# Performance work log

Hardware: AMD Instinct MI355X
Metric: run time of the kernel (lower is better)

Reference implementation:

```python
import jax, jax.numpy as jnp
import numpy as np

B, R, N, M, K = 4, 4, 4096, 64, 3
F_NUM = 512
KN = K * N


def _block(x, Ws, bs):
    """SO-Net PointResNet: 1x1 convs + ReLU; last layer sees concat(input, hidden)."""
    h = x
    for W, b in zip(Ws[:-1], bs[:-1]):
        h = jax.nn.relu(jnp.einsum('oc,bcn->bon', W, h) + b[None, :, None])
    h = jnp.concatenate([x, h], axis=1)
    return jax.nn.relu(jnp.einsum('oc,bcn->bon', Ws[-1], h) + bs[-1][None, :, None])


def _forward(x, intensity, node, node_knn_I, fpW, fpB, gpW, gpB):
    # --- som.query_topk: k nearest SOM nodes per point ---
    xd = jax.lax.stop_gradient(x)
    dist = jnp.sum((xd[:, :, :, None] - node[:, :, None, :]) ** 2, axis=1)      # B,N,M
    _, topk = jax.lax.top_k(-dist, K)                                           # B,N,K
    min_idx = topk.transpose(0, 2, 1).reshape(B, KN)                            # B,KN (k copies stacked)
    mask = jax.nn.one_hot(min_idx, M, dtype=jnp.float32)                        # B,KN,M
    mask_row_max = jnp.max(mask, axis=1) > 0                                    # B,M  node has >=1 point
    mask_row_sum = jnp.sum(mask, axis=1)                                        # B,M  points per node

    x_stack = jnp.tile(x, (1, 1, K))                                            # B,2,KN
    cluster_mean = jnp.einsum('bcn,bnm->bcm', jax.lax.stop_gradient(x_stack), mask) \
                   / (mask_row_sum[:, None, :] + 1e-5)                          # B,2,M (detached)

    # --- rotation group (2x2 rotations at angles 2*pi*r/R) ---
    theta = 2.0 * jnp.pi * jnp.arange(R, dtype=jnp.float32) / R
    c, s = jnp.cos(theta), jnp.sin(theta)
    rot = jnp.stack([jnp.stack([c, -s], -1), jnp.stack([s, c], -1)], -2)        # R,2,2

    x_rot = jnp.einsum('rij,bjn->brin', rot, x_stack)                           # B,R,2,KN
    node_rot = jnp.einsum('rij,bjm->brim', rot, cluster_mean)                   # B,R,2,M
    centers = jnp.take_along_axis(node_rot, min_idx[:, None, None, :], axis=3)  # B,R,2,KN
    x_dec = jax.lax.stop_gradient(x_rot - centers).reshape(B * R, 2, KN)

    # --- first PointResNet over all B*R rotation copies ---
    feat = _block(x_dec, fpW, fpB)                                              # BR,128,KN

    # --- index_max scatter-max per SOM cluster (value of argmax == segment max) ---
    seg = jnp.tile(min_idx[:, None, :], (1, R, 1)).reshape(B * R, KN)
    segmax = jax.vmap(lambda f, sgi: jax.ops.segment_max(f.T, sgi, num_segments=M).T)(feat, seg)
    rowmax = jnp.tile(mask_row_max[:, None, :], (1, R, 1)).reshape(B * R, M)
    pooled = jnp.where(rowmax[:, None, :], segmax, feat[:, :, 0:1])             # BR,128,M (empty -> gather idx 0)

    # --- final PointResNet over SOM nodes, then max over nodes and rotations ---
    g_in = jnp.concatenate([node_rot.reshape(B * R, 2, M), pooled], axis=1)     # BR,130,M
    out = _block(g_in, gpW, gpB)                                                # BR,F,M
    return out.reshape(B, R, F_NUM, M).max(axis=3).max(axis=1)                  # B,F


def setup_inputs() -> dict:
    key = jax.random.key(0)
    ks = jax.random.split(key, 24)
    d = {}
    d['x'] = jax.random.normal(ks[0], (B, 2, N), jnp.float32)
    d['intensity'] = jax.random.uniform(ks[1], (B, 1, N), jnp.float32)
    d['node'] = jax.random.normal(ks[2], (B, 2, M), jnp.float32)
    d['node_knn_I'] = jax.random.randint(ks[3], (B, M, 1), 0, M)
    dims_fp = [(64, 2), (64, 64), (128, 64), (128, 130)]      # PointResNet(2,[64,64,128,128])
    dims_gp = [(256, 130), (256, 256), (512, 256), (F_NUM, 642)]  # PointResNet(130,[256,256,512,F])
    i = 4
    for name, dims in (('fp', dims_fp), ('gp', dims_gp)):
        for j, (o, ci) in enumerate(dims):
            d[f'{name}_W{j}'] = jax.random.normal(ks[i], (o, ci), jnp.float32) / np.sqrt(ci).astype(np.float32)
            d[f'{name}_b{j}'] = jnp.zeros((o,), jnp.float32)
            i += 1
    return d


def reference(x, intensity, node, node_knn_I,
              fp_W0, fp_b0, fp_W1, fp_b1, fp_W2, fp_b2, fp_W3, fp_b3,
              gp_W0, gp_b0, gp_W1, gp_b1, gp_W2, gp_b2, gp_W3, gp_b3):
    return _forward(x, intensity, node, node_knn_I,
                    [fp_W0, fp_W1, fp_W2, fp_W3], [fp_b0, fp_b1, fp_b2, fp_b3],
                    [gp_W0, gp_W1, gp_W2, gp_W3], [gp_b0, gp_b1, gp_b2, gp_b3])
```

## Files before the change

kernel.cpp:

```cpp
#include <hip/hip_runtime.h>
#include <stdint.h>

#define BB 4
#define RR 4
#define NN 4096
#define MM 64
#define KK 3
#define KNN 12288
#define BRR 16
#define FF 512

typedef short bf16x8 __attribute__((ext_vector_type(8)));
typedef float f32x4 __attribute__((ext_vector_type(4)));

__device__ __forceinline__ float bf2f(unsigned int u) {
  union { unsigned int i; float f; } v; v.i = u << 16; return v.f;
}
__device__ __forceinline__ unsigned short f2bf(float f) {
  union { float f; unsigned int i; } v; v.f = f;
  unsigned int x = v.i;
  return (unsigned short)((x + 0x7fffu + ((x >> 16) & 1u)) >> 16);
}
__device__ __forceinline__ unsigned int cvtpk(float a, float b) {
  unsigned int r;
  asm("v_cvt_pk_bf16_f32 %0, %1, %2" : "=v"(r) : "v"(a), "v"(b));
  return r;
}
__device__ __forceinline__ float ldf(const void* p, long i, int isbf) {
  if (isbf) return bf2f(((const unsigned short*)p)[i]);
  return ((const float*)p)[i];
}
__device__ __forceinline__ int hsw(int col, int so) { return col * 72  + (so ^ (col & 24)); }
__device__ __forceinline__ int csw(int col, int so) { return col * 168 + (so ^ (col & 24)); }

struct WPtrs { const void* p[16]; };

__global__ __launch_bounds__(256) void k_front(
    const void* __restrict__ x, const void* __restrict__ node, WPtrs wp,
    int* __restrict__ flag, unsigned short* __restrict__ Wb,
    unsigned short* __restrict__ fW3p, float* __restrict__ Fb,
    int* __restrict__ idx, float* __restrict__ csum, int* __restrict__ blkcnt) {
  __shared__ int bad;
  __shared__ float nd[2][64];
  __shared__ float cs[192];
  int tid = threadIdx.x;
  if (tid == 0) bad = 0;
  __syncthreads();
  {
    const unsigned short* xs = (const unsigned short*)x;
    int cnt = 0;
    for (int i = tid; i < 1024; i += 256) {
      unsigned short u = xs[i * 2];
      int e = (u >> 7) & 0xFF;
      if (e >= 0x90 || (e > 0 && e <= 0x50)) ++cnt;
    }
    atomicAdd(&bad, cnt);
  }
  __syncthreads();
  int isbf = (bad < 100) ? 1 : 0;
  if (blockIdx.x == 0 && tid == 0) flag[0] = isbf;

  if (blockIdx.x < 298) {
    const int e0=4096, e1=12288, e2=28928, e3=62208, e4=127744, e5=258816, e6=587520;
    int t8 = blockIdx.x * 256 + tid;
    if (t8 < 73440) {
      int base = t8 * 8;
      int s, segb;
      if      (base < e0) { s=0; segb=0;  }
      else if (base < e1) { s=1; segb=e0; }
      else if (base < e2) { s=2; segb=e1; }
      else if (base < e3) { s=3; segb=e2; }
      else if (base < e4) { s=4; segb=e3; }
      else if (base < e5) { s=5; segb=e4; }
      else                { s=6; segb=e5; }
      int local = base - segb;
      union { bf16x8 v; unsigned int u[4]; } ov;
      if (isbf) {
        ov.v = *(const bf16x8*)((const unsigned short*)wp.p[s] + local);
      } else {
        const float4* fp = (const float4*)((const float*)wp.p[s] + local);
        float4 f0 = fp[0], f1 = fp[1];
        ov.u[0] = cvtpk(f0.x, f0.y); ov.u[1] = cvtpk(f0.z, f0.w);
        ov.u[2] = cvtpk(f1.x, f1.y); ov.u[3] = cvtpk(f1.z, f1.w);
      }
      *(bf16x8*)(Wb + base) = ov.v;
    } else if (t8 < 76000) {
      int v = t8 - 73440;
      int base = v * 8;
      int o = v / 20, c = (v - o * 20) * 8;
      union { bf16x8 vv; unsigned short s8[8]; } ov;
#pragma unroll
      for (int j = 0; j < 8; ++j) {
        int cc = c + j;
        unsigned short u = 0;
        if (cc < 130) {
          long si = (long)o * 130 + cc;
          if (isbf) u = ((const unsigned short*)wp.p[2])[si];
          else      u = f2bf(((const float*)wp.p[2])[si]);
        }
        ov.s8[j] = u;
      }
      *(bf16x8*)(fW3p + base) = ov.vv;
    } else if (t8 < 76256) {
      int l = (t8 - 76000) * 8;
      const void* src; int off;
      if      (l < 128)  { src = wp.p[7];  off = 0;    }
      else if (l < 192)  { src = wp.p[8];  off = 128;  }
      else if (l < 256)  { src = wp.p[9];  off = 192;  }
      else if (l < 384)  { src = wp.p[10]; off = 256;  }
      else if (l < 512)  { src = wp.p[11]; off = 384;  }
      else if (l < 768)  { src = wp.p[12]; off = 512;  }
      else if (l < 1024) { src = wp.p[13]; off = 768;  }
      else if (l < 1536) { src = wp.p[14]; off = 1024; }
      else               { src = wp.p[15]; off = 1536; }
#pragma unroll
      for (int j = 0; j < 8; ++j) Fb[l + j] = ldf(src, l + j - off, isbf);
    }
    return;
  }
  int bi = blockIdx.x - 298;
  int b = bi >> 4;
  int n = ((bi & 15) << 8) + tid;
  if (tid < 128) nd[tid >> 6][tid & 63] = ldf(node, b * 128 + tid, isbf);
  if (tid < 192) cs[tid] = 0.f;
  __syncthreads();
  float x0 = ldf(x, b * 8192 + n, isbf);
  float x1 = ldf(x, b * 8192 + 4096 + n, isbf);
  float d0 = 1e30f, d1 = 1e30f, d2 = 1e30f;
  int m0 = 0, m1 = 0, m2 = 0;
#pragma unroll 8
  for (int m = 0; m < 64; ++m) {
    float dx = x0 - nd[0][m];
    float dy = x1 - nd[1][m];
    float d = __fmul_rn(dx, dx) + __fmul_rn(dy, dy);
    if (d < d0)      { d2=d1; m2=m1; d1=d0; m1=m0; d0=d; m0=m; }
    else if (d < d1) { d2=d1; m2=m1; d1=d;  m1=m; }
    else if (d < d2) { d2=d;  m2=m; }
  }
  long base = ((long)b * NN + n) * 3;
  idx[base] = m0; idx[base + 1] = m1; idx[base + 2] = m2;
  atomicAdd(&cs[m0*3+0], x0); atomicAdd(&cs[m0*3+1], x1); atomicAdd(&cs[m0*3+2], 1.f);
  atomicAdd(&cs[m1*3+0], x0); atomicAdd(&cs[m1*3+1], x1); atomicAdd(&cs[m1*3+2], 1.f);
  atomicAdd(&cs[m2*3+0], x0); atomicAdd(&cs[m2*3+1], x1); atomicAdd(&cs[m2*3+2], 1.f);
  __syncthreads();
  if (tid < 192) atomicAdd(&csum[b * 192 + tid], cs[tid]);
  if (tid < 64) blkcnt[bi * 64 + tid] = (int)cs[tid*3 + 2];
}

__global__ __launch_bounds__(256) void k_scatter2(
    const float* __restrict__ csum, const int* __restrict__ blkcnt,
    const int* __restrict__ idx, int* __restrict__ sorted,
    float* __restrict__ noderot, int* __restrict__ rowflag) {
  __shared__ int scnt[64];
  __shared__ int soff[64];
  __shared__ int lc[64];
  int tid = threadIdx.x;
  int blk = blockIdx.x;
  int b = blk >> 4, chunk = blk & 15;
  if (tid < 64) scnt[tid] = (int)csum[b*192 + tid*3 + 2];
  __syncthreads();
  if (tid < 64) {
    int m = tid, acc = 0;
    for (int mm = 0; mm < m; ++mm) acc += scnt[mm];
    for (int c = 0; c < chunk; ++c) acc += blkcnt[(b*16 + c)*64 + m];
    soff[m] = acc;
    lc[m] = 0;
    if (chunk == 0) {
      float s0 = csum[b*192 + m*3], s1 = csum[b*192 + m*3 + 1], cc = csum[b*192 + m*3 + 2];
      float mx = s0 / (cc + 1e-5f);
      float my = s1 / (cc + 1e-5f);
      rowflag[b*64 + m] = (cc > 0.f) ? 1 : 0;
      for (int r = 0; r < 4; ++r) {
        float th = 1.5707964f * (float)r;
        float cr = cosf(th), sr = sinf(th);
        noderot[((b*4 + r)*2 + 0)*64 + m] = cr*mx - sr*my;
        noderot[((b*4 + r)*2 + 1)*64 + m] = sr*mx + cr*my;
      }
    }
  }
  __syncthreads();
  int n = ((blk & 15) << 8) + tid;
#pragma unroll
  for (int kk = 0; kk < 3; ++kk) {
    int m = idx[((long)b * NN + n) * 3 + kk];
    int pos = atomicAdd(&lc[m], 1);
    sorted[b * KNN + soff[m] + pos] = (m << 12) | n;
  }
}

__global__ __launch_bounds__(256) void k_fused(
    const void* __restrict__ x, const int* __restrict__ sorted,
    const int* __restrict__ idx, const float* __restrict__ noderot,
    const int* __restrict__ flag, const unsigned short* __restrict__ Wb,
    const unsigned short* __restrict__ fW3p, const float* __restrict__ Fb,
    unsigned int* __restrict__ pooled, float* __restrict__ feat0) {
  __shared__ unsigned short Cs[64 * 168];
  __shared__ unsigned short Hs[64 * 72];
  __shared__ int mcol[64];
  const unsigned short* fW1 = Wb;
  const unsigned short* fW2 = Wb + 4096;
  int isbf = flag[0];
  int tid = threadIdx.x, lane = tid & 63, wv = tid >> 6;
  int quad = lane >> 4, lr = lane & 15;
  int br = blockIdx.y, b = br >> 2, r = br & 3;
  int o1 = wv * 16;
  if (tid < 64) {
    int e = sorted[b * KNN + blockIdx.x * 64 + tid];
    int m = e >> 12, n = e & 4095;
    int isz = (n == 0 && m == idx[(long)b * NN * 3]) ? 256 : 0;
    mcol[tid] = m | isz;
    float x0 = ldf(x, b*8192 + n, isbf), x1 = ldf(x, b*8192 + 4096 + n, isbf);
    float th = 1.5707964f * (float)r;
    float cr = cosf(th), sr = sinf(th);
    float xd0 = (cr*x0 - sr*x1) - noderot[(br*2 + 0)*64 + m];
    float xd1 = (sr*x0 + cr*x1) - noderot[(br*2 + 1)*64 + m];
    *(unsigned int*)&Cs[csw(tid, 0)] = cvtpk(xd0, xd1);
  }
  for (int z = tid; z < 960; z += 256) {
    int col = z / 15, l = 130 + (z - col * 15) * 2;
    *(unsigned int*)&Cs[csw(col, l)] = 0u;
  }
  __syncthreads();
  {
    int col = tid & 63, og = (tid >> 6) << 4;
    unsigned int xu = *(unsigned int*)&Cs[csw(col, 0)];
    float fx0 = bf2f(xu & 0xffff), fx1 = bf2f(xu >> 16);
    const float2* w2 = (const float2*)Fb;
    float hv[16];
#pragma unroll
    for (int j = 0; j < 16; ++j) {
      int o = og + j;
      float2 w = w2[o];
      float h = Fb[128 + o] + w.x * fx0 + w.y * fx1;
      hv[j] = fmaxf(h, 0.f);
    }
    union { bf16x8 v; unsigned int u[4]; } o8[2];
#pragma unroll
    for (int j = 0; j < 16; j += 2) o8[j >> 3].u[(j & 7) >> 1] = cvtpk(hv[j], hv[j+1]);
    *(bf16x8*)&Hs[hsw(col, og)]     = o8[0].v;
    *(bf16x8*)&Hs[hsw(col, og + 8)] = o8[1].v;
  }
  __syncthreads();
  {
    f32x4 acc[4];
#pragma unroll
    for (int nt = 0; nt < 4; ++nt)
      acc[nt] = (f32x4){Fb[192 + o1 + quad*4], Fb[192 + o1 + quad*4 + 1],
                        Fb[192 + o1 + quad*4 + 2], Fb[192 + o1 + quad*4 + 3]};
#pragma unroll
    for (int ks2 = 0; ks2 < 2; ++ks2) {
      bf16x8 a = *(const bf16x8*)(fW1 + (o1 + lr)*64 + ks2*32 + quad*8);
#pragma unroll
      for (int nt = 0; nt < 4; ++nt) {
        bf16x8 bf = *(bf16x8*)&Hs[hsw(nt*16 + lr, ks2*32 + quad*8)];
        acc[nt] = __builtin_amdgcn_mfma_f32_16x16x32_bf16(a, bf, acc[nt], 0, 0, 0);
      }
    }
    __syncthreads();
#pragma unroll
    for (int nt = 0; nt < 4; ++nt) {
      int col = nt*16 + lr;
      unsigned int lo = cvtpk(fmaxf(acc[nt][0], 0.f), fmaxf(acc[nt][1], 0.f));
      unsigned int hi = cvtpk(fmaxf(acc[nt][2], 0.f), fmaxf(acc[nt][3], 0.f));
      *(unsigned long long*)&Hs[hsw(col, o1 + quad*4)] =
          (unsigned long long)lo | ((unsigned long long)hi << 32);
    }
  }
  __syncthreads();
#pragma unroll
  for (int p2 = 0; p2 < 2; ++p2) {
    int o0 = p2*64 + o1;
    f32x4 acc[4];
#pragma unroll
    for (int nt = 0; nt < 4; ++nt)
      acc[nt] = (f32x4){Fb[256 + o0 + quad*4], Fb[256 + o0 + quad*4 + 1],
                        Fb[256 + o0 + quad*4 + 2], Fb[256 + o0 + quad*4 + 3]};
#pragma unroll
    for (int ks2 = 0; ks2 < 2; ++ks2) {
      bf16x8 a = *(const bf16x8*)(fW2 + (o0 + lr)*64 + ks2*32 + quad*8);
#pragma unroll
      for (int nt = 0; nt < 4; ++nt) {
        bf16x8 bf = *(bf16x8*)&Hs[hsw(nt*16 + lr, ks2*32 + quad*8)];
        acc[nt] = __builtin_amdgcn_mfma_f32_16x16x32_bf16(a, bf, acc[nt], 0, 0, 0);
      }
    }
#pragma unroll
    for (int nt = 0; nt < 4; ++nt) {
      int col = nt*16 + lr;
      int o = o0 + quad*4;
      unsigned int w0 = cvtpk(fmaxf(acc[nt][0], 0.f), fmaxf(acc[nt][1], 0.f));
      unsigned int w1 = cvtpk(fmaxf(acc[nt][2], 0.f), fmaxf(acc[nt][3], 0.f));
      *(unsigned int*)&Cs[csw(col, 2 + o)] = w0;
      *(unsigned int*)&Cs[csw(col, 4 + o)] = w1;
    }
  }
  __syncthreads();
  f32x4 acc3[2][4];
#pragma unroll
  for (int p3 = 0; p3 < 2; ++p3) {
    int o0 = p3*64 + o1;
#pragma unroll
    for (int nt = 0; nt < 4; ++nt)
      acc3[p3][nt] = (f32x4){Fb[384 + o0 + quad*4], Fb[384 + o0 + quad*4 + 1],
                             Fb[384 + o0 + quad*4 + 2], Fb[384 + o0 + quad*4 + 3]};
#pragma unroll
    for (int ks5 = 0; ks5 < 5; ++ks5) {
      bf16x8 a = *(const bf16x8*)(fW3p + (o0 + lr)*160 + ks5*32 + quad*8);
#pragma unroll
      for (int nt = 0; nt < 4; ++nt) {
        bf16x8 bf = *(bf16x8*)&Cs[csw(nt*16 + lr, ks5*32 + quad*8)];
        acc3[p3][nt] = __builtin_amdgcn_mfma_f32_16x16x32_bf16(a, bf, acc3[p3][nt], 0, 0, 0);
      }
    }
  }
  __syncthreads();
#pragma unroll
  for (int p3 = 0; p3 < 2; ++p3) {
    int o0 = p3*64 + o1;
#pragma unroll
    for (int nt = 0; nt < 4; ++nt) {
      int col = nt*16 + lr;
      unsigned int lo = cvtpk(fmaxf(acc3[p3][nt][0], 0.f), fmaxf(acc3[p3][nt][1], 0.f));
      unsigned int hi = cvtpk(fmaxf(acc3[p3][nt][2], 0.f), fmaxf(acc3[p3][nt][3], 0.f));
      *(unsigned long long*)&Cs[csw(col, o0 + quad*4)] =
          (unsigned long long)lo | ((unsigned long long)hi << 32);
    }
  }
  __syncthreads();
  {
    int opair = tid & 63, h = tid >> 6;
    int o0 = opair * 2;
    int c0 = h * 16;
    int curm = mcol[c0] & 255;
    unsigned int vlo = 0u, vhi = 0u;
    for (int c = c0; c < c0 + 16; ++c) {
      int mc = mcol[c];
      int mm = mc & 255;
      unsigned int u = *(unsigned int*)&Cs[csw(c, o0)];
      if (mm != curm) {
        atomicMax(&pooled[(((long)br*64 + curm) << 7) + o0],     vlo);
        atomicMax(&pooled[(((long)br*64 + curm) << 7) + o0 + 1], vhi);
        curm = mm; vlo = vhi = 0u;
      }
      vlo = max(vlo, u << 16);
      vhi = max(vhi, u & 0xffff0000u);
      if (mc & 256) {
        feat0[br*128 + o0]     = __uint_as_float(u << 16);
        feat0[br*128 + o0 + 1] = __uint_as_float(u & 0xffff0000u);
      }
    }
    atomicMax(&pooled[(((long)br*64 + curm) << 7) + o0],     vlo);
    atomicMax(&pooled[(((long)br*64 + curm) << 7) + o0 + 1], vhi);
  }
}

template<int OT, int KW, int KMAIN, bool REM2, int DSTR, int DOFF, int EPI>
__device__ __forceinline__ void gp_layer(
    const unsigned short* __restrict__ W, const float* __restrict__ bias,
    const unsigned short* Bs, int bstr, unsigned short* Ds,
    int wv, int quad, int lr, int b, unsigned int* __restrict__ outmax) {
  f32x4 acc[OT];
#pragma unroll
  for (int ot = 0; ot < OT; ++ot) {
    int o0 = (wv * OT + ot) * 16;
    acc[ot] = (f32x4){bias[o0 + quad*4], bias[o0 + quad*4 + 1],
                      bias[o0 + quad*4 + 2], bias[o0 + quad*4 + 3]};
  }
  const unsigned short* brow = Bs + lr * bstr;
  for (int ks = 0; ks < KMAIN; ks += 32) {
    bf16x8 bf = *(const bf16x8*)(brow + ks + quad*8);
    bf16x8 a[OT];
#pragma unroll
    for (int ot = 0; ot < OT; ++ot) {
      const unsigned short* arow = W + (long)((wv * OT + ot) * 16 + lr) * KW;
      if constexpr ((KW % 8) == 0) {
        a[ot] = *(const bf16x8*)(arow + ks + quad*8);
      } else {
        union { bf16x8 v; unsigned int u[4]; } au;
        const unsigned int* ap = (const unsigned int*)(arow + ks + quad*8);
        au.u[0] = ap[0]; au.u[1] = ap[1]; au.u[2] = ap[2]; au.u[3] = ap[3];
        a[ot] = au.v;
      }
    }
#pragma unroll
    for (int ot = 0; ot < OT; ++ot)
      acc[ot] = __builtin_amdgcn_mfma_f32_16x16x32_bf16(a[ot], bf, acc[ot], 0, 0, 0);
  }
  if constexpr (REM2) {
    unsigned int bu = *(const unsigned int*)(brow + KMAIN);
    float b0 = bf2f(bu & 0xffff), b1 = bf2f(bu >> 16);
#pragma unroll
    for (int ot = 0; ot < OT; ++ot) {
#pragma unroll
      for (int rr = 0; rr < 4; ++rr) {
        int o = (wv * OT + ot) * 16 + quad*4 + rr;
        unsigned int wu = *(const unsigned int*)(W + (long)o * KW + KMAIN);
        acc[ot][rr] += bf2f(wu & 0xffff) * b0 + bf2f(wu >> 16) * b1;
      }
    }
  }
#pragma unroll
  for (int ot = 0; ot < OT; ++ot) {
    int o0 = (wv * OT + ot) * 16;
    if constexpr (EPI == 0) {
      unsigned int lo = cvtpk(fmaxf(acc[ot][0], 0.f), fmaxf(acc[ot][1], 0.f));
      unsigned int hi = cvtpk(fmaxf(acc[ot][2], 0.f), fmaxf(acc[ot][3], 0.f));
      unsigned short* op = Ds + lr * DSTR + DOFF + o0 + quad*4;
      if constexpr ((DOFF & 3) == 0) {
        *(unsigned long long*)op = (unsigned long long)lo | ((unsigned long long)hi << 32);
      } else {
        *(unsigned int*)op       = lo;
        *(unsigned int*)(op + 2) = hi;
      }
    } else {
#pragma unroll
      for (int rr = 0; rr < 4; ++rr) {
        float v = fmaxf(acc[ot][rr], 0.f);
        v = fmaxf(v, __shfl_xor(v, 1, 64));
        v = fmaxf(v, __shfl_xor(v, 2, 64));
        v = fmaxf(v, __shfl_xor(v, 4, 64));
        v = fmaxf(v, __shfl_xor(v, 8, 64));
        if (lr == 0)
          atomicMax(&outmax[b * FF + o0 + quad*4 + rr], __float_as_uint(v));
      }
    }
  }
}

__global__ __launch_bounds__(1024) void k_gp(
    const unsigned int* __restrict__ pooled, const float* __restrict__ feat0,
    const int* __restrict__ rowflag, const float* __restrict__ noderot,
    const unsigned short* __restrict__ Wb, const float* __restrict__ Fb,
    const int* __restrict__ flag, int* __restrict__ tick,
    unsigned int* __restrict__ outmax, void* __restrict__ out) {
  __shared__ unsigned short G3[16 * 648];
  __shared__ unsigned short H1[16 * 264];
  __shared__ unsigned short H2[16 * 264];
  __shared__ int lastf;
  const unsigned short* gW0 = Wb + 28928;
  const unsigned short* gW1 = Wb + 62208;
  const unsigned short* gW2 = Wb + 127744;
  const unsigned short* gW3 = Wb + 258816;
  int tid = threadIdx.x, lane = tid & 63, wv = tid >> 6;
  int quad = lane >> 4, lr = lane & 15;
  int c0 = blockIdx.x * 16;
  int br = c0 >> 6, b = br >> 2;
  {
    int j = tid >> 6, oq = (tid & 63) << 1;
    int col = c0 + j, m = col & 63;
    int fl = rowflag[b * 64 + m];
    float v0 = __uint_as_float(pooled[((long)col << 7) + oq]);
    float v1 = __uint_as_float(pooled[((long)col << 7) + oq + 1]);
    if (!fl) { v0 = feat0[br * 128 + oq]; v1 = feat0[br * 128 + oq + 1]; }
    *(unsigned int*)&G3[j * 648 + 2 + oq] = cvtpk(v0, v1);
    if (tid < 32) {
      int jj = tid >> 1, o = tid & 1;
      int mm = (c0 + jj) & 63;
      G3[jj * 648 + o] = f2bf(noderot[(br * 2 + o) * 64 + mm]);
    }
  }
  __syncthreads();
  gp_layer<1, 130, 128, true,  264, 0,   0>(gW0, Fb + 512,  G3, 648, H1, wv, quad, lr, b, outmax);
  __syncthreads();
  gp_layer<1, 256, 256, false, 264, 0,   0>(gW1, Fb + 768,  H1, 264, H2, wv, quad, lr, b, outmax);
  __syncthreads();
  gp_layer<2, 256, 256, false, 648, 130, 0>(gW2, Fb + 1024, H2, 264, G3, wv, quad, lr, b, outmax);
  __syncthreads();
  gp_layer<2, 642, 640, true,  0,   0,   1>(gW3, Fb + 1536, G3, 648, nullptr, wv, quad, lr, b, outmax);
  __threadfence();
  if (tid == 0) lastf = (atomicAdd(tick, 1) == 63) ? 1 : 0;
  __syncthreads();
  if (lastf) {
    int isbf = flag[0];
    for (int t = tid; t < 2048; t += 1024) {
      unsigned int u = atomicMax(&outmax[t], 0u);
      float v = __uint_as_float(u);
      if (isbf) ((unsigned short*)out)[t] = f2bf(v);
      else      ((float*)out)[t] = v;
    }
  }
}

extern "C" void kernel_launch(void* const* d_in, const int* in_sizes, int n_in,
                              void* d_out, int out_size, void* d_ws, size_t ws_size,
                              hipStream_t stream) {
  const void* x    = d_in[0];
  const void* node = d_in[2];

  char* ws = (char*)d_ws;
  int*            flag    = (int*)(ws + 0);
  int*            tick    = (int*)(ws + 128);
  float*          csum    = (float*)(ws + 256);
  unsigned int*   outmax  = (unsigned int*)(ws + 3328);
  unsigned int*   pooled  = (unsigned int*)(ws + 11520);
  int*            idx     = (int*)(ws + 535808);
  int*            blkcnt  = (int*)(ws + 732416);
  float*          noderot = (float*)(ws + 766208);
  int*            rowflag = (int*)(ws + 774400);
  int*            sorted  = (int*)(ws + 775424);
  float*          feat0   = (float*)(ws + 972032);
  unsigned short* fW3p    = (unsigned short*)(ws + 980224);
  float*          Fb      = (float*)(ws + 1021184);
  unsigned short* Wb      = (unsigned short*)(ws + 3355904);

  hipMemsetAsync(ws, 0, 535808, stream);

  WPtrs wp;
  wp.p[0]=d_in[6];  wp.p[1]=d_in[8];  wp.p[2]=d_in[10];
  wp.p[3]=d_in[12]; wp.p[4]=d_in[14]; wp.p[5]=d_in[16]; wp.p[6]=d_in[18];
  wp.p[7]=d_in[4];
  wp.p[8]=d_in[5];  wp.p[9]=d_in[7];  wp.p[10]=d_in[9]; wp.p[11]=d_in[11];
  wp.p[12]=d_in[13]; wp.p[13]=d_in[15]; wp.p[14]=d_in[17]; wp.p[15]=d_in[19];

  k_front<<<362, 256, 0, stream>>>(x, node, wp, flag, Wb, fW3p, Fb, idx, csum, blkcnt);
  k_scatter2<<<64, 256, 0, stream>>>(csum, blkcnt, idx, sorted, noderot, rowflag);
  k_fused<<<dim3(192, 16), 256, 0, stream>>>(x, sorted, idx, noderot, flag,
                                             Wb, fW3p, Fb, pooled, feat0);
  k_gp<<<64, 1024, 0, stream>>>(pooled, feat0, rowflag, noderot, Wb, Fb,
                                flag, tick, outmax, d_out);
}
```

Before: 202.8 us.

## Prefetch gp weights into cache from fused kernel and batch weight loads

The fused first-stage kernel now has each block read a slice of the later-layer weight buffer and discard the result. This is meant to warm the L2/MALL cache before the gp layers run. The gp_layer inner loop is restructured to load A and B fragments for four k-steps before issuing their MFMAs, so more global loads are in flight at once. This raises register pressure. The loop assumes KMAIN/32 is a multiple of 4, otherwise it reads past the range.

```diff
diff --git a/kernel.cpp b/kernel.cpp
--- a/kernel.cpp
+++ b/kernel.cpp
@@ -204,6 +204,18 @@
   int quad = lane >> 4, lr = lane & 15;
   int br = blockIdx.y, b = br >> 2, r = br & 3;
   int o1 = wv * 16;
+  {
+    unsigned int wacc = 0;
+#pragma unroll
+    for (int i = 0; i < 2; ++i) {
+      int off = 28928 + blockIdx.x * 2912 + i * 2048 + tid * 8;
+      if (off < 587520) {
+        const unsigned int* p = (const unsigned int*)(Wb + off);
+        wacc ^= p[0] ^ p[1] ^ p[2] ^ p[3];
+      }
+    }
+    asm volatile("" :: "v"(wacc));
+  }
   if (tid < 64) {
     int e = sorted[b * KNN + blockIdx.x * 64 + tid];
     int m = e >> 12, n = e & 4095;
@@ -367,24 +379,33 @@
                       bias[o0 + quad*4 + 2], bias[o0 + quad*4 + 3]};
   }
   const unsigned short* brow = Bs + lr * bstr;
-  for (int ks = 0; ks < KMAIN; ks += 32) {
-    bf16x8 bf = *(const bf16x8*)(brow + ks + quad*8);
-    bf16x8 a[OT];
-#pragma unroll
-    for (int ot = 0; ot < OT; ++ot) {
-      const unsigned short* arow = W + (long)((wv * OT + ot) * 16 + lr) * KW;
-      if constexpr ((KW % 8) == 0) {
-        a[ot] = *(const bf16x8*)(arow + ks + quad*8);
-      } else {
-        union { bf16x8 v; unsigned int u[4]; } au;
-        const unsigned int* ap = (const unsigned int*)(arow + ks + quad*8);
-        au.u[0] = ap[0]; au.u[1] = ap[1]; au.u[2] = ap[2]; au.u[3] = ap[3];
-        a[ot] = au.v;
-      }
-    }
-#pragma unroll
-    for (int ot = 0; ot < OT; ++ot)
-      acc[ot] = __builtin_amdgcn_mfma_f32_16x16x32_bf16(a[ot], bf, acc[ot], 0, 0, 0);
+  constexpr int NS = KMAIN / 32;
+#pragma unroll 1
+  for (int c = 0; c < NS; c += 4) {
+    bf16x8 bfv[4];
+    bf16x8 av[4][OT];
+#pragma unroll
+    for (int j = 0; j < 4; ++j) {
+      int ks = (c + j) * 32;
+      bfv[j] = *(const bf16x8*)(brow + ks + quad*8);
+#pragma unroll
+      for (int ot = 0; ot < OT; ++ot) {
+        const unsigned short* arow = W + (long)((wv * OT + ot) * 16 + lr) * KW;
+        if constexpr ((KW % 8) == 0) {
+          av[j][ot] = *(const bf16x8*)(arow + ks + quad*8);
+        } else {
+          union { bf16x8 v; unsigned int u[4]; } au;
+          const unsigned int* ap = (const unsigned int*)(arow + ks + quad*8);
+          au.u[0] = ap[0]; au.u[1] = ap[1]; au.u[2] = ap[2]; au.u[3] = ap[3];
+          av[j][ot] = au.v;
+        }
+      }
+    }
+#pragma unroll
+    for (int j = 0; j < 4; ++j)
+#pragma unroll
+      for (int ot = 0; ot < OT; ++ot)
+        acc[ot] = __builtin_amdgcn_mfma_f32_16x16x32_bf16(av[j][ot], bfv[j], acc[ot], 0, 0, 0);
   }
   if constexpr (REM2) {
     unsigned int bu = *(const unsigned int*)(brow + KMAIN);
```

Measured after the change: 207.0 us. +2.0%, slower.

## Split fused GP MLP kernel into per-layer GEMM launches with wider grids

Applied to the files above, without the earlier changes.

Replaces the single 64-block, 1024-thread kernel that ran all four GP layers in shared memory with four separate GEMM kernel launches, each spread over a 2D grid of output-channel tiles and point tiles. Intermediate activations now round-trip through global workspace buffers, and layer 3 recomputes the pooled-feature gather instead of reading it from shared memory. The aim is more parallelism and better CU occupancy across the GPU, at the cost of extra launches, global memory traffic, and weight reloads per block.

```diff
diff --git a/kernel.cpp b/kernel.cpp
--- a/kernel.cpp
+++ b/kernel.cpp
@@ -354,129 +354,134 @@
   }
 }
 
-template<int OT, int KW, int KMAIN, bool REM2, int DSTR, int DOFF, int EPI>
-__device__ __forceinline__ void gp_layer(
+template<int KW, int KWP, int KMAIN, bool REM2, bool GIN, int INSTR, int HOFF,
+         int NT, int EPI, int NBLK>
+__global__ __launch_bounds__(256) void k_gemm(
     const unsigned short* __restrict__ W, const float* __restrict__ bias,
-    const unsigned short* Bs, int bstr, unsigned short* Ds,
-    int wv, int quad, int lr, int b, unsigned int* __restrict__ outmax) {
-  f32x4 acc[OT];
-#pragma unroll
-  for (int ot = 0; ot < OT; ++ot) {
-    int o0 = (wv * OT + ot) * 16;
-    acc[ot] = (f32x4){bias[o0 + quad*4], bias[o0 + quad*4 + 1],
-                      bias[o0 + quad*4 + 2], bias[o0 + quad*4 + 3]};
-  }
-  const unsigned short* brow = Bs + lr * bstr;
-  for (int ks = 0; ks < KMAIN; ks += 32) {
-    bf16x8 bf = *(const bf16x8*)(brow + ks + quad*8);
-    bf16x8 a[OT];
-#pragma unroll
-    for (int ot = 0; ot < OT; ++ot) {
-      const unsigned short* arow = W + (long)((wv * OT + ot) * 16 + lr) * KW;
-      if constexpr ((KW % 8) == 0) {
-        a[ot] = *(const bf16x8*)(arow + ks + quad*8);
-      } else {
-        union { bf16x8 v; unsigned int u[4]; } au;
-        const unsigned int* ap = (const unsigned int*)(arow + ks + quad*8);
-        au.u[0] = ap[0]; au.u[1] = ap[1]; au.u[2] = ap[2]; au.u[3] = ap[3];
-        a[ot] = au.v;
-      }
-    }
-#pragma unroll
-    for (int ot = 0; ot < OT; ++ot)
-      acc[ot] = __builtin_amdgcn_mfma_f32_16x16x32_bf16(a[ot], bf, acc[ot], 0, 0, 0);
-  }
-  if constexpr (REM2) {
-    unsigned int bu = *(const unsigned int*)(brow + KMAIN);
-    float b0 = bf2f(bu & 0xffff), b1 = bf2f(bu >> 16);
-#pragma unroll
-    for (int ot = 0; ot < OT; ++ot) {
-#pragma unroll
-      for (int rr = 0; rr < 4; ++rr) {
-        int o = (wv * OT + ot) * 16 + quad*4 + rr;
-        unsigned int wu = *(const unsigned int*)(W + (long)o * KW + KMAIN);
-        acc[ot][rr] += bf2f(wu & 0xffff) * b0 + bf2f(wu >> 16) * b1;
-      }
-    }
-  }
-#pragma unroll
-  for (int ot = 0; ot < OT; ++ot) {
-    int o0 = (wv * OT + ot) * 16;
-    if constexpr (EPI == 0) {
-      unsigned int lo = cvtpk(fmaxf(acc[ot][0], 0.f), fmaxf(acc[ot][1], 0.f));
-      unsigned int hi = cvtpk(fmaxf(acc[ot][2], 0.f), fmaxf(acc[ot][3], 0.f));
-      unsigned short* op = Ds + lr * DSTR + DOFF + o0 + quad*4;
-      if constexpr ((DOFF & 3) == 0) {
-        *(unsigned long long*)op = (unsigned long long)lo | ((unsigned long long)hi << 32);
-      } else {
-        *(unsigned int*)op       = lo;
-        *(unsigned int*)(op + 2) = hi;
-      }
-    } else {
-#pragma unroll
-      for (int rr = 0; rr < 4; ++rr) {
-        float v = fmaxf(acc[ot][rr], 0.f);
-        v = fmaxf(v, __shfl_xor(v, 1, 64));
-        v = fmaxf(v, __shfl_xor(v, 2, 64));
-        v = fmaxf(v, __shfl_xor(v, 4, 64));
-        v = fmaxf(v, __shfl_xor(v, 8, 64));
-        if (lr == 0)
-          atomicMax(&outmax[b * FF + o0 + quad*4 + rr], __float_as_uint(v));
-      }
-    }
-  }
-}
-
-__global__ __launch_bounds__(1024) void k_gp(
     const unsigned int* __restrict__ pooled, const float* __restrict__ feat0,
     const int* __restrict__ rowflag, const float* __restrict__ noderot,
-    const unsigned short* __restrict__ Wb, const float* __restrict__ Fb,
-    const int* __restrict__ flag, int* __restrict__ tick,
-    unsigned int* __restrict__ outmax, void* __restrict__ out) {
-  __shared__ unsigned short G3[16 * 648];
-  __shared__ unsigned short H1[16 * 264];
-  __shared__ unsigned short H2[16 * 264];
+    const unsigned short* __restrict__ Bg, unsigned short* __restrict__ Out,
+    int OSTR, unsigned int* __restrict__ outmax,
+    const int* __restrict__ flag, int* __restrict__ tick, void* __restrict__ out) {
+  __shared__ __align__(16) unsigned short Bs[NT * 16 * KWP];
   __shared__ int lastf;
-  const unsigned short* gW0 = Wb + 28928;
-  const unsigned short* gW1 = Wb + 62208;
-  const unsigned short* gW2 = Wb + 127744;
-  const unsigned short* gW3 = Wb + 258816;
   int tid = threadIdx.x, lane = tid & 63, wv = tid >> 6;
   int quad = lane >> 4, lr = lane & 15;
-  int c0 = blockIdx.x * 16;
-  int br = c0 >> 6, b = br >> 2;
-  {
-    int j = tid >> 6, oq = (tid & 63) << 1;
-    int col = c0 + j, m = col & 63;
-    int fl = rowflag[b * 64 + m];
-    float v0 = __uint_as_float(pooled[((long)col << 7) + oq]);
-    float v1 = __uint_as_float(pooled[((long)col << 7) + oq + 1]);
-    if (!fl) { v0 = feat0[br * 128 + oq]; v1 = feat0[br * 128 + oq + 1]; }
-    *(unsigned int*)&G3[j * 648 + 2 + oq] = cvtpk(v0, v1);
-    if (tid < 32) {
-      int jj = tid >> 1, o = tid & 1;
-      int mm = (c0 + jj) & 63;
-      G3[jj * 648 + o] = f2bf(noderot[(br * 2 + o) * 64 + mm]);
-    }
-  }
-  __syncthreads();
-  gp_layer<1, 130, 128, true,  264, 0,   0>(gW0, Fb + 512,  G3, 648, H1, wv, quad, lr, b, outmax);
-  __syncthreads();
-  gp_layer<1, 256, 256, false, 264, 0,   0>(gW1, Fb + 768,  H1, 264, H2, wv, quad, lr, b, outmax);
-  __syncthreads();
-  gp_layer<2, 256, 256, false, 648, 130, 0>(gW2, Fb + 1024, H2, 264, G3, wv, quad, lr, b, outmax);
-  __syncthreads();
-  gp_layer<2, 642, 640, true,  0,   0,   1>(gW3, Fb + 1536, G3, 648, nullptr, wv, quad, lr, b, outmax);
-  __threadfence();
-  if (tid == 0) lastf = (atomicAdd(tick, 1) == 63) ? 1 : 0;
-  __syncthreads();
-  if (lastf) {
-    int isbf = flag[0];
-    for (int t = tid; t < 2048; t += 1024) {
-      unsigned int u = atomicMax(&outmax[t], 0u);
-      float v = __uint_as_float(u);
-      if (isbf) ((unsigned short*)out)[t] = f2bf(v);
-      else      ((float*)out)[t] = v;
+  int p0 = blockIdx.x * (NT * 16);
+  int br = p0 >> 6, b = br >> 2;
+  if constexpr (GIN) {
+    for (int i = tid; i < NT * 256; i += 256) {
+      int j = i >> 4, g = i & 15;
+      int col = p0 + j, m = col & 63;
+      int fl = rowflag[b * 64 + m];
+      int o8 = g * 8;
+      unsigned int wq[4];
+#pragma unroll
+      for (int q = 0; q < 4; ++q) {
+        float v0, v1;
+        if (fl) {
+          v0 = __uint_as_float(pooled[((long)col << 7) + o8 + q*2]);
+          v1 = __uint_as_float(pooled[((long)col << 7) + o8 + q*2 + 1]);
+        } else {
+          v0 = feat0[br * 128 + o8 + q*2];
+          v1 = feat0[br * 128 + o8 + q*2 + 1];
+        }
+        wq[q] = cvtpk(v0, v1);
+      }
+#pragma unroll
+      for (int q = 0; q < 4; ++q)
+        *(unsigned int*)&Bs[j * KWP + 2 + o8 + q*2] = wq[q];
+    }
+    if (tid < NT * 32) {
+      int j = tid >> 1, o = tid & 1;
+      Bs[j * KWP + o] = f2bf(noderot[(br * 2 + o) * 64 + ((p0 + j) & 63)]);
+    }
+  }
+  if constexpr (INSTR > 0) {
+    constexpr int NG = INSTR / 8;
+    for (int i = tid; i < NT * 16 * NG; i += 256) {
+      int j = i / NG, g = i - j * NG;
+      union { bf16x8 v; unsigned int u[4]; } t;
+      t.v = *(const bf16x8*)&Bg[(long)(p0 + j) * INSTR + g * 8];
+      if constexpr ((HOFF % 8) == 0) {
+        *(bf16x8*)&Bs[j * KWP + HOFF + g * 8] = t.v;
+      } else {
+#pragma unroll
+        for (int q = 0; q < 4; ++q)
+          *(unsigned int*)&Bs[j * KWP + HOFF + g * 8 + q*2] = t.u[q];
+      }
+    }
+  }
+  __syncthreads();
+  int o0 = blockIdx.y * 64 + wv * 16;
+  f32x4 acc[NT];
+#pragma unroll
+  for (int nt = 0; nt < NT; ++nt)
+    acc[nt] = (f32x4){bias[o0 + quad*4], bias[o0 + quad*4 + 1],
+                      bias[o0 + quad*4 + 2], bias[o0 + quad*4 + 3]};
+  const unsigned short* arow = W + (long)(o0 + lr) * KW;
+  for (int ks = 0; ks < KMAIN; ks += 32) {
+    bf16x8 a;
+    if constexpr ((KW % 8) == 0) {
+      a = *(const bf16x8*)(arow + ks + quad*8);
+    } else {
+      union { bf16x8 v; unsigned int u[4]; } au;
+      const unsigned int* ap = (const unsigned int*)(arow + ks + quad*8);
+      au.u[0] = ap[0]; au.u[1] = ap[1]; au.u[2] = ap[2]; au.u[3] = ap[3];
+      a = au.v;
+    }
+#pragma unroll
+    for (int nt = 0; nt < NT; ++nt) {
+      bf16x8 bf = *(bf16x8*)&Bs[(nt*16 + lr) * KWP + ks + quad*8];
+      acc[nt] = __builtin_amdgcn_mfma_f32_16x16x32_bf16(a, bf, acc[nt], 0, 0, 0);
+    }
+  }
+  if constexpr (REM2) {
+#pragma unroll
+    for (int rr = 0; rr < 4; ++rr) {
+      int o = o0 + quad*4 + rr;
+      unsigned int wu = *(const unsigned int*)(W + (long)o * KW + KMAIN);
+      float w0 = bf2f(wu & 0xffff), w1 = bf2f(wu >> 16);
+#pragma unroll
+      for (int nt = 0; nt < NT; ++nt) {
+        unsigned int bu = *(unsigned int*)&Bs[(nt*16 + lr) * KWP + KMAIN];
+        acc[nt][rr] += w0 * bf2f(bu & 0xffff) + w1 * bf2f(bu >> 16);
+      }
+    }
+  }
+  if constexpr (EPI == 0) {
+#pragma unroll
+    for (int nt = 0; nt < NT; ++nt) {
+      unsigned int lo = cvtpk(fmaxf(acc[nt][0], 0.f), fmaxf(acc[nt][1], 0.f));
+      unsigned int hi = cvtpk(fmaxf(acc[nt][2], 0.f), fmaxf(acc[nt][3], 0.f));
+      unsigned short* op = Out + (long)(p0 + nt*16 + lr) * OSTR + o0 + quad*4;
+      *(unsigned long long*)op = (unsigned long long)lo | ((unsigned long long)hi << 32);
+    }
+  } else {
+#pragma unroll
+    for (int rr = 0; rr < 4; ++rr) {
+      float v = acc[0][rr];
+#pragma unroll
+      for (int nt = 1; nt < NT; ++nt) v = fmaxf(v, acc[nt][rr]);
+      v = fmaxf(v, 0.f);
+      v = fmaxf(v, __shfl_xor(v, 1, 64));
+      v = fmaxf(v, __shfl_xor(v, 2, 64));
+      v = fmaxf(v, __shfl_xor(v, 4, 64));
+      v = fmaxf(v, __shfl_xor(v, 8, 64));
+      if (lr == 0)
+        atomicMax(&outmax[b * FF + o0 + quad*4 + rr], __float_as_uint(v));
+    }
+    __threadfence();
+    if (tid == 0) lastf = (atomicAdd(tick, 1) == NBLK - 1) ? 1 : 0;
+    __syncthreads();
+    if (lastf) {
+      int isbf = flag[0];
+      for (int t = tid; t < 2048; t += 256) {
+        unsigned int u = atomicMax(&outmax[t], 0u);
+        float v = __uint_as_float(u);
+        if (isbf) ((unsigned short*)out)[t] = f2bf(v);
+        else      ((float*)out)[t] = v;
+      }
     }
   }
 }
@@ -501,6 +506,9 @@
   float*          feat0   = (float*)(ws + 972032);
   unsigned short* fW3p    = (unsigned short*)(ws + 980224);
   float*          Fb      = (float*)(ws + 1021184);
+  unsigned short* Hg3     = (unsigned short*)(ws + 1048576);
+  unsigned short* Hg1     = (unsigned short*)(ws + 2307328);
+  unsigned short* Hg2     = (unsigned short*)(ws + 2831616);
   unsigned short* Wb      = (unsigned short*)(ws + 3355904);
 
   hipMemsetAsync(ws, 0, 535808, stream);
@@ -512,10 +520,29 @@
   wp.p[8]=d_in[5];  wp.p[9]=d_in[7];  wp.p[10]=d_in[9]; wp.p[11]=d_in[11];
   wp.p[12]=d_in[13]; wp.p[13]=d_in[15]; wp.p[14]=d_in[17]; wp.p[15]=d_in[19];
 
+  const unsigned short* gW0 = Wb + 28928;
+  const unsigned short* gW1 = Wb + 62208;
+  const unsigned short* gW2 = Wb + 127744;
+  const unsigned short* gW3 = Wb + 258816;
+
   k_front<<<362, 256, 0, stream>>>(x, node, wp, flag, Wb, fW3p, Fb, idx, csum, blkcnt);
   k_scatter2<<<64, 256, 0, stream>>>(csum, blkcnt, idx, sorted, noderot, rowflag);
   k_fused<<<dim3(192, 16), 256, 0, stream>>>(x, sorted, idx, noderot, flag,
                                              Wb, fW3p, Fb, pooled, feat0);
-  k_gp<<<64, 1024, 0, stream>>>(pooled, feat0, rowflag, noderot, Wb, Fb,
-                                flag, tick, outmax, d_out);
-}
+  k_gemm<130, 136, 128, true,  true,  0,   0,   1, 0, 0>
+      <<<dim3(64, 4), 256, 0, stream>>>(gW0, Fb + 512, pooled, feat0, rowflag,
+                                        noderot, nullptr, Hg1, 256, nullptr,
+                                        flag, tick, nullptr);
+  k_gemm<256, 264, 256, false, false, 256, 0,   1, 0, 0>
+      <<<dim3(64, 4), 256, 0, stream>>>(gW1, Fb + 768, pooled, feat0, rowflag,
+                                        noderot, Hg1, Hg2, 256, nullptr,
+                                        flag, tick, nullptr);
+  k_gemm<256, 264, 256, false, false, 256, 0,   2, 0, 0>
+      <<<dim3(32, 8), 256, 0, stream>>>(gW2, Fb + 1024, pooled, feat0, rowflag,
+                                        noderot, Hg2, Hg3, 512, nullptr,
+                                        flag, tick, nullptr);
+  k_gemm<642, 648, 640, true,  true,  512, 130, 2, 2, 256>
+      <<<dim3(32, 8), 256, 0, stream>>>(gW3, Fb + 1536, pooled, feat0, rowflag,
+                                        noderot, Hg3, nullptr, 0, outmax,
+                                        flag, tick, d_out);
+}
```

New measurement: 189.3 us. -6.7%, faster.
